# Performance work log

Hardware: AMD Instinct MI355X
Metric: run time of the kernel (lower is better)

Reference implementation:

```python
import jax, jax.numpy as jnp
import numpy as np

N = 100000
E = 1600000
IN = 128
HID = 128
OUT = 64


def sage_conv(x, src, dst, deg_inv, W_l, b_l, W_r):
    # PyG SAGEConv (mean aggr): out = lin_l(mean_{j in N(i)} x_j) + lin_r(x_i)
    msgs = x[src]                                   # [E, F] gather
    agg = jax.ops.segment_sum(msgs, dst, num_segments=N)  # [N, F]
    agg = agg * deg_inv[:, None]                    # mean
    return agg @ W_l + b_l + x @ W_r


def setup_inputs() -> dict:
    key = jax.random.key(0)
    ks = jax.random.split(key, 9)
    x = jax.random.normal(ks[0], (N, IN), dtype=jnp.float32)
    edge_index = jax.random.randint(ks[1], (2, E), 0, N, dtype=jnp.int64)
    s = 1.0 / np.sqrt(IN)
    W1l = jax.random.uniform(ks[2], (IN, HID), jnp.float32, -s, s)
    b1 = jax.random.uniform(ks[3], (HID,), jnp.float32, -s, s)
    W1r = jax.random.uniform(ks[4], (IN, HID), jnp.float32, -s, s)
    s2 = 1.0 / np.sqrt(HID)
    W2l = jax.random.uniform(ks[5], (HID, HID), jnp.float32, -s2, s2)
    b2 = jax.random.uniform(ks[6], (HID,), jnp.float32, -s2, s2)
    W2r = jax.random.uniform(ks[7], (HID, HID), jnp.float32, -s2, s2)
    kl1, kl2 = jax.random.split(ks[8])
    Wlin = jax.random.uniform(kl1, (HID, OUT), jnp.float32, -s2, s2)
    blin = jax.random.uniform(kl2, (OUT,), jnp.float32, -s2, s2)
    return {"x": x, "edge_index": edge_index, "W1l": W1l, "b1": b1, "W1r": W1r,
            "W2l": W2l, "b2": b2, "W2r": W2r, "Wlin": Wlin, "blin": blin}


def reference(x, edge_index, W1l, b1, W1r, W2l, b2, W2r, Wlin, blin):
    src, dst = edge_index[0], edge_index[1]
    deg = jax.ops.segment_sum(jnp.ones((E,), jnp.float32), dst, num_segments=N)
    deg_inv = 1.0 / jnp.maximum(deg, 1.0)
    h = sage_conv(x, src, dst, deg_inv, W1l, b1, W1r)
    h = jax.nn.relu(h)
    # dropout: training=False -> identity
    h2 = sage_conv(h, src, dst, deg_inv, W2l, b2, W2r)
    h = jax.nn.relu(h + h2)
    return h @ Wlin + blin
```

## Files before the change

kernel.cpp:

```cpp
#include <hip/hip_runtime.h>
#include <hip/hip_bf16.h>
#include <cstdint>

#define NND 100000
#define NED 1600000
#define FIN 128
#define FOUT 64

typedef __bf16 bf16x8 __attribute__((ext_vector_type(8)));
typedef float f32x4 __attribute__((ext_vector_type(4)));

static __device__ inline unsigned short f2bf(float f) {
    unsigned int u = __builtin_bit_cast(unsigned int, f);
    unsigned int r = (u + 0x7fffu + ((u >> 16) & 1u)) >> 16;
    return (unsigned short)r;
}
static __device__ inline float bflo(unsigned int v) {
    return __builtin_bit_cast(float, v << 16);
}
static __device__ inline float bfhi(unsigned int v) {
    return __builtin_bit_cast(float, v & 0xffff0000u);
}
static __device__ inline float bf1(unsigned short u) {
    return __builtin_bit_cast(float, (unsigned int)u << 16);
}

__global__ __launch_bounds__(256) void k_deg_cast(const int* __restrict__ dst,
                                                  int* __restrict__ deg,
                                                  int* __restrict__ rank, int e,
                                                  const float* __restrict__ x,
                                                  unsigned int* __restrict__ xb,
                                                  int total2) {
    int i = blockIdx.x * 256 + threadIdx.x;
    if (i < e) rank[i] = atomicAdd(&deg[dst[i]], 1);
    if (i < total2) {
        float2 v = ((const float2*)x)[i];
        xb[i] = (unsigned int)f2bf(v.x) | ((unsigned int)f2bf(v.y) << 16);
    }
}

__global__ __launch_bounds__(1024) void k_scan1(const int* __restrict__ deg,
                                                int* __restrict__ psum, int n) {
    __shared__ int red[1024];
    int tid = threadIdx.x;
    int i = blockIdx.x * 1024 + tid;
    red[tid] = (i < n) ? deg[i] : 0;
    __syncthreads();
#pragma unroll
    for (int off = 512; off > 0; off >>= 1) {
        if (tid < off) red[tid] += red[tid + off];
        __syncthreads();
    }
    if (tid == 0) psum[blockIdx.x] = red[0];
}

__global__ __launch_bounds__(128) void k_scan2(int* __restrict__ psum, int nb) {
    int tid = threadIdx.x;
    int d = (tid < nb) ? psum[tid] : 0;
    int v = d;
#pragma unroll
    for (int off = 1; off < 64; off <<= 1) {
        int u = __shfl_up(v, off, 64);
        if ((tid & 63) >= off) v += u;
    }
    __shared__ int ws[2];
    if ((tid & 63) == 63) ws[tid >> 6] = v;
    __syncthreads();
    int base = (tid >= 64) ? ws[0] : 0;
    if (tid < nb) psum[tid] = base + v - d;
}

__global__ __launch_bounds__(1024) void k_scan3(const int* __restrict__ deg,
                                                const int* __restrict__ psum,
                                                int* __restrict__ offs,
                                                float* __restrict__ dinv,
                                                int n, int e) {
    int tid = threadIdx.x;
    int i = blockIdx.x * 1024 + tid;
    int d = (i < n) ? deg[i] : 0;
    int v = d;
#pragma unroll
    for (int off = 1; off < 64; off <<= 1) {
        int u = __shfl_up(v, off, 64);
        if ((tid & 63) >= off) v += u;
    }
    __shared__ int wsum[16];
    int wid = tid >> 6;
    if ((tid & 63) == 63) wsum[wid] = v;
    __syncthreads();
    if (tid < 16) {
        int w = wsum[tid];
#pragma unroll
        for (int off = 1; off < 16; off <<= 1) {
            int u = __shfl_up(w, off, 64);
            if (tid >= off) w += u;
        }
        wsum[tid] = w;
    }
    __syncthreads();
    int base = psum[blockIdx.x] + (wid ? wsum[wid - 1] : 0);
    if (i < n) {
        offs[i] = base + v - d;
        dinv[i] = 1.0f / fmaxf((float)d, 1.0f);
    }
    if (i == 0) offs[n] = e;
}

__global__ __launch_bounds__(256) void k_csr(const int* __restrict__ src,
                                             const int* __restrict__ dst,
                                             const int* __restrict__ rank,
                                             const int* __restrict__ offs,
                                             int* __restrict__ csr, int e) {
    int i = blockIdx.x * 256 + threadIdx.x;
    if (i < e) {
        csr[offs[dst[i]] + rank[i]] = src[i];
    }
}

static __device__ inline void pack_one(const float* __restrict__ W,
                                       unsigned short* __restrict__ out,
                                       int NTtot, int c_local, int nt,
                                       int chunkOff, int ncols, int lane) {
    int k = c_local * 32 + (lane >> 4) * 8;
    int n = nt * 16 + (lane & 15);
    unsigned short t[8];
#pragma unroll
    for (int j = 0; j < 8; j++) t[j] = f2bf(W[(size_t)(k + j) * ncols + n]);
    uint4 u;
    u.x = t[0] | ((unsigned)t[1] << 16);
    u.y = t[2] | ((unsigned)t[3] << 16);
    u.z = t[4] | ((unsigned)t[5] << 16);
    u.w = t[6] | ((unsigned)t[7] << 16);
    *(uint4*)&out[((size_t)((c_local + chunkOff) * NTtot + nt) * 64 + lane) * 8] = u;
}

__global__ __launch_bounds__(64) void k_packAll(const float* W1l, const float* W1r,
                                                const float* W2l, const float* W2r,
                                                const float* Wlin,
                                                unsigned short* p1, unsigned short* p2,
                                                unsigned short* ph) {
    int b = blockIdx.x, lane = threadIdx.x;
    if (b < 32)       pack_one(W1l, p1, 8, b >> 3, b & 7, 0, 128, lane);
    else if (b < 64)  { b -= 32; pack_one(W1r, p1, 8, b >> 3, b & 7, 4, 128, lane); }
    else if (b < 96)  { b -= 64; pack_one(W2l, p2, 8, b >> 3, b & 7, 0, 128, lane); }
    else if (b < 128) { b -= 96; pack_one(W2r, p2, 8, b >> 3, b & 7, 4, 128, lane); }
    else              { b -= 128; pack_one(Wlin, ph, 4, b >> 2, b & 3, 0, 64, lane); }
}

#define ACC8(v) do { \
    acc[0].x += bflo((v).x); acc[0].y += bfhi((v).x); \
    acc[1].x += bflo((v).y); acc[1].y += bfhi((v).y); \
    acc[2].x += bflo((v).z); acc[2].y += bfhi((v).z); \
    acc[3].x += bflo((v).w); acc[3].y += bfhi((v).w); } while (0)

__global__ __launch_bounds__(256) void k_aggb(const uint4* __restrict__ feat4,
                                              const int* __restrict__ offs,
                                              const int* __restrict__ csr,
                                              const float* __restrict__ dinv,
                                              uint4* __restrict__ out4, int n) {
    int node = blockIdx.x * 4 + (threadIdx.x >> 6);
    if (node >= n) return;
    int lane = threadIdx.x & 63;
    int grp = lane >> 4;
    int ch = lane & 15;
    int beg = offs[node], end = offs[node + 1];
    int deg = end - beg;

    float2 acc[4];
#pragma unroll
    for (int j = 0; j < 4; j++) acc[j] = make_float2(0.f, 0.f);

    int i = beg;
    int fullEnd = beg + (deg & ~15);
    for (; i < fullEnd; i += 16) {
        int s0 = csr[i + grp];
        int s1 = csr[i + 4 + grp];
        int s2 = csr[i + 8 + grp];
        int s3 = csr[i + 12 + grp];
        uint4 v0 = feat4[(size_t)s0 * 16 + ch];
        uint4 v1 = feat4[(size_t)s1 * 16 + ch];
        uint4 v2 = feat4[(size_t)s2 * 16 + ch];
        uint4 v3 = feat4[(size_t)s3 * 16 + ch];
        ACC8(v0); ACC8(v1); ACC8(v2); ACC8(v3);
    }
    if (i < end) {
#pragma unroll
        for (int g = 0; g < 4; g++) {
            int e = i + g * 4 + grp;
            bool p = e < end;
            int s = csr[p ? e : beg];
            uint4 v = feat4[(size_t)s * 16 + ch];
            if (p) { ACC8(v); }
        }
    }
#pragma unroll
    for (int j = 0; j < 4; j++) {
        acc[j].x += __shfl_xor(acc[j].x, 16);
        acc[j].y += __shfl_xor(acc[j].y, 16);
        acc[j].x += __shfl_xor(acc[j].x, 32);
        acc[j].y += __shfl_xor(acc[j].y, 32);
    }
    if (grp == 0) {
        float di = dinv[node];
        uint4 o;
        o.x = (unsigned)f2bf(acc[0].x * di) | ((unsigned)f2bf(acc[0].y * di) << 16);
        o.y = (unsigned)f2bf(acc[1].x * di) | ((unsigned)f2bf(acc[1].y * di) << 16);
        o.z = (unsigned)f2bf(acc[2].x * di) | ((unsigned)f2bf(acc[2].y * di) << 16);
        o.w = (unsigned)f2bf(acc[3].x * di) | ((unsigned)f2bf(acc[3].y * di) << 16);
        out4[(size_t)node * 16 + ch] = o;
    }
}

template <int NT, int KCH, bool TWO, bool RELU, bool RESID, bool HEAD, bool OUTBF>
__global__ __launch_bounds__(256) void k_mfma(const unsigned short* __restrict__ P,
                                              const unsigned short* __restrict__ Q,
                                              const unsigned short* __restrict__ Wp,
                                              const float* __restrict__ bias,
                                              const unsigned short* __restrict__ resid,
                                              const unsigned short* __restrict__ Wp2,
                                              const float* __restrict__ bias2,
                                              void* __restrict__ outv, int n) {
    const int lane = threadIdx.x & 63;
    const int wave = threadIdx.x >> 6;
    const int quad = lane >> 4;
    const int row0 = blockIdx.x * 64 + wave * 16;
    int rowA = row0 + (lane & 15);
    if (rowA >= n) rowA = n - 1;

    f32x4 acc[NT];
#pragma unroll
    for (int t = 0; t < NT; t++) acc[t] = (f32x4){0.f, 0.f, 0.f, 0.f};

#pragma unroll
    for (int c = 0; c < KCH; c++) {
        const unsigned short* Abase = (TWO && c >= KCH / 2) ? Q : P;
        const int kk = (TWO ? (c & (KCH / 2 - 1)) : c) * 32 + quad * 8;
        bf16x8 a = *(const bf16x8*)&Abase[(size_t)rowA * 128 + kk];
#pragma unroll
        for (int t = 0; t < NT; t++) {
            bf16x8 b = *(const bf16x8*)&Wp[(size_t)((c * NT + t) * 64 + lane) * 8];
            acc[t] = __builtin_amdgcn_mfma_f32_16x16x32_bf16(a, b, acc[t], 0, 0, 0);
        }
    }

    const int col = lane & 15;
    if (!HEAD) {
#pragma unroll
        for (int t = 0; t < NT; t++) {
            float bv = bias[t * 16 + col];
#pragma unroll
            for (int r = 0; r < 4; r++) {
                int row = row0 + quad * 4 + r;
                if (row < n) {
                    float v = acc[t][r] + bv;
                    if (RESID) v += bf1(resid[(size_t)row * 128 + t * 16 + col]);
                    if (RELU) v = fmaxf(v, 0.f);
                    if (OUTBF)
                        ((unsigned short*)outv)[(size_t)row * (NT * 16) + t * 16 + col] = f2bf(v);
                    else
                        ((float*)outv)[(size_t)row * (NT * 16) + t * 16 + col] = v;
                }
            }
        }
    } else {
        __shared__ __align__(16) unsigned short sT[4][16 * 136];
#pragma unroll
        for (int t = 0; t < NT; t++) {
            float bv = bias[t * 16 + col];
#pragma unroll
            for (int r = 0; r < 4; r++) {
                int row = row0 + quad * 4 + r;
                int rr = row < n ? row : n - 1;
                float v = acc[t][r] + bv;
                if (RESID) v += bf1(resid[(size_t)rr * 128 + t * 16 + col]);
                if (RELU) v = fmaxf(v, 0.f);
                sT[wave][(quad * 4 + r) * 136 + t * 16 + col] = f2bf(v);
            }
        }
        f32x4 hacc[4];
#pragma unroll
        for (int t = 0; t < 4; t++) hacc[t] = (f32x4){0.f, 0.f, 0.f, 0.f};
#pragma unroll
        for (int c = 0; c < 4; c++) {
            bf16x8 a = *(const bf16x8*)&sT[wave][(lane & 15) * 136 + c * 32 + quad * 8];
#pragma unroll
            for (int t = 0; t < 4; t++) {
                bf16x8 b = *(const bf16x8*)&Wp2[(size_t)((c * 4 + t) * 64 + lane) * 8];
                hacc[t] = __builtin_amdgcn_mfma_f32_16x16x32_bf16(a, b, hacc[t], 0, 0, 0);
            }
        }
#pragma unroll
        for (int t = 0; t < 4; t++) {
            float bv = bias2[t * 16 + col];
#pragma unroll
            for (int r = 0; r < 4; r++) {
                int row = row0 + quad * 4 + r;
                if (row < n)
                    ((float*)outv)[(size_t)row * 64 + t * 16 + col] = hacc[t][r] + bv;
            }
        }
    }
}

extern "C" void kernel_launch(void* const* d_in, const int* in_sizes, int n_in,
                              void* d_out, int out_size, void* d_ws, size_t ws_size,
                              hipStream_t stream) {
    const float* x    = (const float*)d_in[0];
    const int*   ei   = (const int*)d_in[1];
    const float* W1l  = (const float*)d_in[2];
    const float* b1   = (const float*)d_in[3];
    const float* W1r  = (const float*)d_in[4];
    const float* W2l  = (const float*)d_in[5];
    const float* b2   = (const float*)d_in[6];
    const float* W2r  = (const float*)d_in[7];
    const float* Wlin = (const float*)d_in[8];
    const float* blin = (const float*)d_in[9];
    float* out = (float*)d_out;

    const int N = NND, E = NED;
    const int* src = ei;
    const int* dst = ei + E;
    const int NB = (N + 1023) / 1024;

    char* w = (char*)d_ws;
    int*   deg    = (int*)w;               w += (size_t)N * 4;
    int*   offs   = (int*)w;               w += (size_t)(N + 4) * 4;
    float* dinv   = (float*)w;             w += (size_t)N * 4;
    int*   psum   = (int*)w;               w += (size_t)((NB + 3) & ~3) * 4;
    int*   rank   = (int*)w;               w += (size_t)E * 4;
    int*   csr    = (int*)w;               w += (size_t)E * 4;
    unsigned short* p1  = (unsigned short*)w;  w += 256 * 128 * 2;
    unsigned short* p2  = (unsigned short*)w;  w += 256 * 128 * 2;
    unsigned short* ph  = (unsigned short*)w;  w += 128 * 64 * 2;
    unsigned short* xb  = (unsigned short*)w;  w += (size_t)N * 128 * 2;
    unsigned short* agg = (unsigned short*)w;  w += (size_t)N * 128 * 2;
    unsigned short* h1  = (unsigned short*)w;  w += (size_t)N * 128 * 2;

    hipMemsetAsync(deg, 0, (size_t)N * 4, stream);

    k_deg_cast<<<(N * 64 + 255) / 256, 256, 0, stream>>>(dst, deg, rank, E, x,
                                                         (unsigned int*)xb, N * 64);
    k_scan1<<<NB, 1024, 0, stream>>>(deg, psum, N);
    k_scan2<<<1, 128, 0, stream>>>(psum, NB);
    k_scan3<<<NB, 1024, 0, stream>>>(deg, psum, offs, dinv, N, E);
    k_csr<<<E / 256, 256, 0, stream>>>(src, dst, rank, offs, csr, E);
    k_packAll<<<144, 64, 0, stream>>>(W1l, W1r, W2l, W2r, Wlin, p1, p2, ph);

    k_aggb<<<(N + 3) / 4, 256, 0, stream>>>((const uint4*)xb, offs, csr, dinv,
                                            (uint4*)agg, N);
    k_mfma<8, 8, true, true, false, false, true><<<(N + 63) / 64, 256, 0, stream>>>(
        agg, xb, p1, b1, nullptr, nullptr, nullptr, h1, N);

    k_aggb<<<(N + 3) / 4, 256, 0, stream>>>((const uint4*)h1, offs, csr, dinv,
                                            (uint4*)agg, N);
    k_mfma<8, 8, true, true, true, true, false><<<(N + 63) / 64, 256, 0, stream>>>(
        agg, h1, p2, b2, h1, ph, blin, out, N);
}
```

Baseline: 443.8 us.

## Build CSR via two-pass bucketed counting sort with shared-memory atomics

Replaces the global per-edge atomic degree count and rank-based CSR scatter with a radix-style build. Edges are first histogrammed into 256 coarse destination buckets per block in LDS, scanned, and scattered into bucket order. A per-bucket kernel then builds node offsets, degree inverses and the final CSR using LDS atomics. Weight packing and the x-to-bf16 cast are folded into the histogram kernel, saving launches and the memset, at the cost of an extra 8-byte-per-edge intermediate buffer and one more pass over the edges.

After: 388.3 us. -12.5%, faster.

```diff
diff --git a/kernel.cpp b/kernel.cpp
--- a/kernel.cpp
+++ b/kernel.cpp
@@ -7,6 +7,13 @@
 #define FIN 128
 #define FOUT 64
 
+#define NBLK 512
+#define EPB (NED / NBLK)
+#define NBUCK 256
+#define BSH 9
+#define BNODES 512
+#define HTN (NBUCK * NBLK)
+
 typedef __bf16 bf16x8 __attribute__((ext_vector_type(8)));
 typedef float f32x4 __attribute__((ext_vector_type(4)));
 
@@ -23,98 +30,6 @@
 }
 static __device__ inline float bf1(unsigned short u) {
     return __builtin_bit_cast(float, (unsigned int)u << 16);
-}
-
-__global__ __launch_bounds__(256) void k_deg_cast(const int* __restrict__ dst,
-                                                  int* __restrict__ deg,
-                                                  int* __restrict__ rank, int e,
-                                                  const float* __restrict__ x,
-                                                  unsigned int* __restrict__ xb,
-                                                  int total2) {
-    int i = blockIdx.x * 256 + threadIdx.x;
-    if (i < e) rank[i] = atomicAdd(&deg[dst[i]], 1);
-    if (i < total2) {
-        float2 v = ((const float2*)x)[i];
-        xb[i] = (unsigned int)f2bf(v.x) | ((unsigned int)f2bf(v.y) << 16);
-    }
-}
-
-__global__ __launch_bounds__(1024) void k_scan1(const int* __restrict__ deg,
-                                                int* __restrict__ psum, int n) {
-    __shared__ int red[1024];
-    int tid = threadIdx.x;
-    int i = blockIdx.x * 1024 + tid;
-    red[tid] = (i < n) ? deg[i] : 0;
-    __syncthreads();
-#pragma unroll
-    for (int off = 512; off > 0; off >>= 1) {
-        if (tid < off) red[tid] += red[tid + off];
-        __syncthreads();
-    }
-    if (tid == 0) psum[blockIdx.x] = red[0];
-}
-
-__global__ __launch_bounds__(128) void k_scan2(int* __restrict__ psum, int nb) {
-    int tid = threadIdx.x;
-    int d = (tid < nb) ? psum[tid] : 0;
-    int v = d;
-#pragma unroll
-    for (int off = 1; off < 64; off <<= 1) {
-        int u = __shfl_up(v, off, 64);
-        if ((tid & 63) >= off) v += u;
-    }
-    __shared__ int ws[2];
-    if ((tid & 63) == 63) ws[tid >> 6] = v;
-    __syncthreads();
-    int base = (tid >= 64) ? ws[0] : 0;
-    if (tid < nb) psum[tid] = base + v - d;
-}
-
-__global__ __launch_bounds__(1024) void k_scan3(const int* __restrict__ deg,
-                                                const int* __restrict__ psum,
-                                                int* __restrict__ offs,
-                                                float* __restrict__ dinv,
-                                                int n, int e) {
-    int tid = threadIdx.x;
-    int i = blockIdx.x * 1024 + tid;
-    int d = (i < n) ? deg[i] : 0;
-    int v = d;
-#pragma unroll
-    for (int off = 1; off < 64; off <<= 1) {
-        int u = __shfl_up(v, off, 64);
-        if ((tid & 63) >= off) v += u;
-    }
-    __shared__ int wsum[16];
-    int wid = tid >> 6;
-    if ((tid & 63) == 63) wsum[wid] = v;
-    __syncthreads();
-    if (tid < 16) {
-        int w = wsum[tid];
-#pragma unroll
-        for (int off = 1; off < 16; off <<= 1) {
-            int u = __shfl_up(w, off, 64);
-            if (tid >= off) w += u;
-        }
-        wsum[tid] = w;
-    }
-    __syncthreads();
-    int base = psum[blockIdx.x] + (wid ? wsum[wid - 1] : 0);
-    if (i < n) {
-        offs[i] = base + v - d;
-        dinv[i] = 1.0f / fmaxf((float)d, 1.0f);
-    }
-    if (i == 0) offs[n] = e;
-}
-
-__global__ __launch_bounds__(256) void k_csr(const int* __restrict__ src,
-                                             const int* __restrict__ dst,
-                                             const int* __restrict__ rank,
-                                             const int* __restrict__ offs,
-                                             int* __restrict__ csr, int e) {
-    int i = blockIdx.x * 256 + threadIdx.x;
-    if (i < e) {
-        csr[offs[dst[i]] + rank[i]] = src[i];
-    }
 }
 
 static __device__ inline void pack_one(const float* __restrict__ W,
@@ -134,17 +49,156 @@
     *(uint4*)&out[((size_t)((c_local + chunkOff) * NTtot + nt) * 64 + lane) * 8] = u;
 }
 
-__global__ __launch_bounds__(64) void k_packAll(const float* W1l, const float* W1r,
-                                                const float* W2l, const float* W2r,
-                                                const float* Wlin,
-                                                unsigned short* p1, unsigned short* p2,
-                                                unsigned short* ph) {
-    int b = blockIdx.x, lane = threadIdx.x;
-    if (b < 32)       pack_one(W1l, p1, 8, b >> 3, b & 7, 0, 128, lane);
-    else if (b < 64)  { b -= 32; pack_one(W1r, p1, 8, b >> 3, b & 7, 4, 128, lane); }
-    else if (b < 96)  { b -= 64; pack_one(W2l, p2, 8, b >> 3, b & 7, 0, 128, lane); }
-    else if (b < 128) { b -= 96; pack_one(W2r, p2, 8, b >> 3, b & 7, 4, 128, lane); }
-    else              { b -= 128; pack_one(Wlin, ph, 4, b >> 2, b & 3, 0, 64, lane); }
+__global__ __launch_bounds__(256) void k_hist_cast(
+        const int* __restrict__ dst, int* __restrict__ histT,
+        const float* __restrict__ x, unsigned int* __restrict__ xb,
+        const float* W1l, const float* W1r, const float* W2l,
+        const float* W2r, const float* Wlin,
+        unsigned short* p1, unsigned short* p2, unsigned short* ph) {
+    __shared__ int hist[NBUCK];
+    const int tid = threadIdx.x, blk = blockIdx.x;
+    hist[tid] = 0;
+    __syncthreads();
+    const int e0 = blk * EPB, e1 = e0 + EPB;
+    for (int i = e0 + tid; i < e1; i += 256)
+        atomicAdd(&hist[dst[i] >> BSH], 1);
+    __syncthreads();
+    histT[tid * NBLK + blk] = hist[tid];
+    if (blk < 144 && tid < 64) {
+        int b = blk, lane = tid;
+        if (b < 32)       pack_one(W1l, p1, 8, b >> 3, b & 7, 0, 128, lane);
+        else if (b < 64)  { b -= 32; pack_one(W1r, p1, 8, b >> 3, b & 7, 4, 128, lane); }
+        else if (b < 96)  { b -= 64; pack_one(W2l, p2, 8, b >> 3, b & 7, 0, 128, lane); }
+        else if (b < 128) { b -= 96; pack_one(W2r, p2, 8, b >> 3, b & 7, 4, 128, lane); }
+        else              { b -= 128; pack_one(Wlin, ph, 4, b >> 2, b & 3, 0, 64, lane); }
+    }
+    const int total2 = NND * 64;
+    for (int i = blk * 256 + tid; i < total2; i += NBLK * 256) {
+        float2 v = ((const float2*)x)[i];
+        xb[i] = (unsigned int)f2bf(v.x) | ((unsigned int)f2bf(v.y) << 16);
+    }
+}
+
+__global__ __launch_bounds__(1024) void g_scan1(const int* __restrict__ in,
+                                                int* __restrict__ psum, int n) {
+    __shared__ int red[1024];
+    int tid = threadIdx.x;
+    int i = blockIdx.x * 1024 + tid;
+    red[tid] = (i < n) ? in[i] : 0;
+    __syncthreads();
+#pragma unroll
+    for (int off = 512; off > 0; off >>= 1) {
+        if (tid < off) red[tid] += red[tid + off];
+        __syncthreads();
+    }
+    if (tid == 0) psum[blockIdx.x] = red[0];
+}
+
+__global__ __launch_bounds__(128) void g_scan2(int* __restrict__ psum, int nb) {
+    int tid = threadIdx.x;
+    int d = (tid < nb) ? psum[tid] : 0;
+    int v = d;
+#pragma unroll
+    for (int off = 1; off < 64; off <<= 1) {
+        int u = __shfl_up(v, off, 64);
+        if ((tid & 63) >= off) v += u;
+    }
+    __shared__ int ws[2];
+    if ((tid & 63) == 63) ws[tid >> 6] = v;
+    __syncthreads();
+    int base = (tid >= 64) ? ws[0] : 0;
+    if (tid < nb) psum[tid] = base + v - d;
+}
+
+__global__ __launch_bounds__(1024) void g_scan3(const int* __restrict__ in,
+                                                const int* __restrict__ psum,
+                                                int* __restrict__ out, int n) {
+    int tid = threadIdx.x;
+    int i = blockIdx.x * 1024 + tid;
+    int d = (i < n) ? in[i] : 0;
+    int v = d;
+#pragma unroll
+    for (int off = 1; off < 64; off <<= 1) {
+        int u = __shfl_up(v, off, 64);
+        if ((tid & 63) >= off) v += u;
+    }
+    __shared__ int wsum[16];
+    int wid = tid >> 6;
+    if ((tid & 63) == 63) wsum[wid] = v;
+    __syncthreads();
+    if (tid < 16) {
+        int w = wsum[tid];
+#pragma unroll
+        for (int off = 1; off < 16; off <<= 1) {
+            int u = __shfl_up(w, off, 64);
+            if (tid >= off) w += u;
+        }
+        wsum[tid] = w;
+    }
+    __syncthreads();
+    int base = psum[blockIdx.x] + (wid ? wsum[wid - 1] : 0);
+    if (i < n) out[i] = base + v - d;
+}
+
+__global__ __launch_bounds__(256) void k_scatter(const int* __restrict__ src,
+                                                 const int* __restrict__ dst,
+                                                 const int* __restrict__ sh,
+                                                 uint2* __restrict__ eS) {
+    __shared__ int cur[NBUCK];
+    const int tid = threadIdx.x, blk = blockIdx.x;
+    cur[tid] = sh[tid * NBLK + blk];
+    __syncthreads();
+    const int e0 = blk * EPB, e1 = e0 + EPB;
+    for (int i = e0 + tid; i < e1; i += 256) {
+        int d = dst[i];
+        int pos = atomicAdd(&cur[d >> BSH], 1);
+        eS[pos] = make_uint2((unsigned)src[i], (unsigned)(d & (BNODES - 1)));
+    }
+}
+
+__global__ __launch_bounds__(1024) void k_bucket(const uint2* __restrict__ eS,
+                                                 const int* __restrict__ sh,
+                                                 int* __restrict__ csr,
+                                                 int* __restrict__ offs,
+                                                 float* __restrict__ dinv, int n) {
+    __shared__ int cnt[BNODES];
+    __shared__ int loc[BNODES];
+    const int b = blockIdx.x, tid = threadIdx.x;
+    const int base = sh[b * NBLK];
+    const int end = (b == NBUCK - 1) ? NED : sh[(b + 1) * NBLK];
+    if (tid < BNODES) cnt[tid] = 0;
+    __syncthreads();
+    for (int i = base + tid; i < end; i += 1024)
+        atomicAdd(&cnt[eS[i].y], 1);
+    __syncthreads();
+    if (tid < BNODES) loc[tid] = cnt[tid];
+    __syncthreads();
+#pragma unroll
+    for (int off = 1; off < BNODES; off <<= 1) {
+        int v = 0;
+        if (tid < BNODES && tid >= off) v = loc[tid - off];
+        __syncthreads();
+        if (tid < BNODES) loc[tid] += v;
+        __syncthreads();
+    }
+    int node = b * BNODES + tid;
+    int myExcl = 0;
+    if (tid < BNODES) {
+        myExcl = loc[tid] - cnt[tid];
+        if (node < n) {
+            offs[node] = base + myExcl;
+            dinv[node] = 1.0f / fmaxf((float)cnt[tid], 1.0f);
+        }
+    }
+    __syncthreads();
+    if (tid < BNODES) cnt[tid] = base + myExcl;
+    __syncthreads();
+    for (int i = base + tid; i < end; i += 1024) {
+        uint2 e = eS[i];
+        int slot = atomicAdd(&cnt[e.y], 1);
+        csr[slot] = (int)e.x;
+    }
+    if (b == 0 && tid == 0) offs[n] = NED;
 }
 
 #define ACC8(v) do { \
@@ -320,14 +374,15 @@
     const int N = NND, E = NED;
     const int* src = ei;
     const int* dst = ei + E;
-    const int NB = (N + 1023) / 1024;
+    const int NB2 = HTN / 1024;
 
     char* w = (char*)d_ws;
-    int*   deg    = (int*)w;               w += (size_t)N * 4;
+    int*   histT  = (int*)w;               w += (size_t)HTN * 4;
+    int*   sh     = (int*)w;               w += (size_t)HTN * 4;
+    int*   psum   = (int*)w;               w += (size_t)NB2 * 4;
     int*   offs   = (int*)w;               w += (size_t)(N + 4) * 4;
     float* dinv   = (float*)w;             w += (size_t)N * 4;
-    int*   psum   = (int*)w;               w += (size_t)((NB + 3) & ~3) * 4;
-    int*   rank   = (int*)w;               w += (size_t)E * 4;
+    uint2* eS     = (uint2*)w;             w += (size_t)E * 8;
     int*   csr    = (int*)w;               w += (size_t)E * 4;
     unsigned short* p1  = (unsigned short*)w;  w += 256 * 128 * 2;
     unsigned short* p2  = (unsigned short*)w;  w += 256 * 128 * 2;
@@ -336,15 +391,13 @@
     unsigned short* agg = (unsigned short*)w;  w += (size_t)N * 128 * 2;
     unsigned short* h1  = (unsigned short*)w;  w += (size_t)N * 128 * 2;
 
-    hipMemsetAsync(deg, 0, (size_t)N * 4, stream);
-
-    k_deg_cast<<<(N * 64 + 255) / 256, 256, 0, stream>>>(dst, deg, rank, E, x,
-                                                         (unsigned int*)xb, N * 64);
-    k_scan1<<<NB, 1024, 0, stream>>>(deg, psum, N);
-    k_scan2<<<1, 128, 0, stream>>>(psum, NB);
-    k_scan3<<<NB, 1024, 0, stream>>>(deg, psum, offs, dinv, N, E);
-    k_csr<<<E / 256, 256, 0, stream>>>(src, dst, rank, offs, csr, E);
-    k_packAll<<<144, 64, 0, stream>>>(W1l, W1r, W2l, W2r, Wlin, p1, p2, ph);
+    k_hist_cast<<<NBLK, 256, 0, stream>>>(dst, histT, x, (unsigned int*)xb,
+                                          W1l, W1r, W2l, W2r, Wlin, p1, p2, ph);
+    g_scan1<<<NB2, 1024, 0, stream>>>(histT, psum, HTN);
+    g_scan2<<<1, 128, 0, stream>>>(psum, NB2);
+    g_scan3<<<NB2, 1024, 0, stream>>>(histT, psum, sh, HTN);
+    k_scatter<<<NBLK, 256, 0, stream>>>(src, dst, sh, eS);
+    k_bucket<<<NBUCK, 1024, 0, stream>>>(eS, sh, csr, offs, dinv, N);
 
     k_aggb<<<(N + 3) / 4, 256, 0, stream>>>((const uint4*)xb, offs, csr, dinv,
                                             (uint4*)agg, N);
```
